# Kernel tuning notes

Hardware: AMD Instinct MI355X
Metric: run time of the kernel (lower is better)

## Reference

```python
import jax, jax.numpy as jnp
import numpy as np

N = 50000   # nodes
E = 800000  # edges
G = 64      # graphs
NEG_SLOPE = 0.2  # PyG GATConv leaky_relu slope


def gat_conv(x, edge_index, edge_attr, W, att_src, att_dst, We, att_edge, bias, num_nodes):
    # PyG GATConv, add_self_loops=False, concat=True, eval (no dropout)
    H, C = att_src.shape
    h = (x @ W).reshape(-1, H, C)                      # [N,H,C]
    a_src = (h * att_src).sum(-1)                      # [N,H]
    a_dst = (h * att_dst).sum(-1)                      # [N,H]
    src, dst = edge_index[0], edge_index[1]
    e = (edge_attr @ We).reshape(-1, H, C)             # [E,H,C]
    a_edge = (e * att_edge).sum(-1)                    # [E,H]
    alpha = a_src[src] + a_dst[dst] + a_edge           # [E,H]
    alpha = jax.nn.leaky_relu(alpha, NEG_SLOPE)
    # segment softmax over incoming edges of each dst node
    amax = jax.ops.segment_max(alpha, dst, num_segments=num_nodes)
    amax = jnp.where(jnp.isfinite(amax), amax, 0.0)
    ex = jnp.exp(alpha - amax[dst])
    denom = jax.ops.segment_sum(ex, dst, num_segments=num_nodes)
    att = ex / (denom[dst] + 1e-16)                    # [E,H]
    msg = h[src] * att[..., None]                      # [E,H,C]
    out = jax.ops.segment_sum(msg, dst, num_segments=num_nodes)
    return out.reshape(num_nodes, H * C) + bias


def setup_inputs() -> dict:
    key = jax.random.key(0)
    ks = jax.random.split(key, 20)
    s = 0.1
    inp = {
        "x": jax.random.normal(ks[0], (N, 128), jnp.float32),
        "edge_index": jax.random.randint(ks[1], (2, E), 0, N, dtype=jnp.int32),
        "edge_attr": jax.random.normal(ks[2], (E, 1), jnp.float32),
        "batch": jnp.sort(jax.random.randint(ks[3], (N,), 0, G, dtype=jnp.int32)),
        # layer 1: 128 -> 4 heads x 32
        "W1": jax.random.normal(ks[4], (128, 128), jnp.float32) * s,
        "as1": jax.random.normal(ks[5], (4, 32), jnp.float32) * s,
        "ad1": jax.random.normal(ks[6], (4, 32), jnp.float32) * s,
        "We1": jax.random.normal(ks[7], (1, 128), jnp.float32) * s,
        "ae1": jax.random.normal(ks[8], (4, 32), jnp.float32) * s,
        "b1": jnp.zeros((128,), jnp.float32),
        # layer 2: 128 -> 1 head x 64
        "W2": jax.random.normal(ks[9], (128, 64), jnp.float32) * s,
        "as2": jax.random.normal(ks[10], (1, 64), jnp.float32) * s,
        "ad2": jax.random.normal(ks[11], (1, 64), jnp.float32) * s,
        "We2": jax.random.normal(ks[12], (1, 64), jnp.float32) * s,
        "ae2": jax.random.normal(ks[13], (1, 64), jnp.float32) * s,
        "b2": jnp.zeros((64,), jnp.float32),
        # prediction head
        "Wp": jax.random.normal(ks[14], (64, 1), jnp.float32) * s,
        "bp": jnp.zeros((1,), jnp.float32),
    }
    return inp


def reference(x, edge_index, edge_attr, batch, W1, as1, ad1, We1, ae1, b1,
              W2, as2, ad2, We2, ae2, b2, Wp, bp):
    h = gat_conv(x, edge_index, edge_attr, W1, as1, ad1, We1, ae1, b1, N)
    h = jax.nn.relu(h)  # dropout p=0.0, eval mode
    h = gat_conv(h, edge_index, edge_attr, W2, as2, ad2, We2, ae2, b2, N)
    # per-graph mean pooling (vectorized replacement of the python loop)
    counts = jax.ops.segment_sum(jnp.ones((N,), h.dtype), batch, num_segments=G)
    sums = jax.ops.segment_sum(h, batch, num_segments=G)   # [G,64]
    mean = sums / counts[:, None]
    out = mean @ Wp + bp                                   # [G,1]
    return out.squeeze(-1)                                 # [G]
```

## Files before the change

### kernel.cpp

```cpp
#include <hip/hip_runtime.h>
#include <hip/hip_bf16.h>

typedef unsigned short u16;
typedef unsigned int u32;

#define MAXB 2048
#define POOL_MAXG 64

typedef __attribute__((ext_vector_type(8))) short bf16x8;
typedef __attribute__((ext_vector_type(4))) float f32x4;

__device__ __forceinline__ float bf2f(u16 u) { return __uint_as_float(((u32)u) << 16); }
__device__ __forceinline__ float bl(u32 u) { return __uint_as_float(u << 16); }
__device__ __forceinline__ float bh(u32 u) { return __uint_as_float(u & 0xffff0000u); }
__device__ __forceinline__ u16 f2bf(float f) {
    u32 u = __float_as_uint(f);
    u += 0x7fffu + ((u >> 16) & 1u);
    return (u16)(u >> 16);
}
__device__ __forceinline__ float lrelu(float x) { return x > 0.f ? x : 0.2f * x; }
__device__ __forceinline__ int clampi(int v, int lo, int hi) {
    return v < lo ? lo : (v > hi ? hi : v);
}
__device__ __forceinline__ float load1(const void* base, int idx, int f32) {
    return f32 ? ((const float*)base)[idx] : bf2f(((const u16*)base)[idx]);
}
__device__ __forceinline__ float cexpf(float a) {
    return __builtin_amdgcn_exp2f(fminf(a, 30.f) * 1.4426950408889634f);
}

__global__ void k_detect(const u32* __restrict__ xw, int* __restrict__ flag,
                         int* __restrict__ bcnt, int B) {
    int lane = threadIdx.x & 63;
    for (int i = lane; i < B; i += 64) bcnt[i] = 0;
    int cnt = 0;
    #pragma unroll
    for (int j = 0; j < 4; j++) {
        u32 w = xw[lane * 4 + j];
        int e0 = (int)((w >> 7) & 0xffu);
        int e1 = (int)((w >> 23) & 0xffu);
        cnt += (e0 >= 0x60 && e0 <= 0x8f);
        cnt += (e1 >= 0x60 && e1 <= 0x8f);
    }
    #pragma unroll
    for (int off = 32; off > 0; off >>= 1) cnt += __shfl_xor(cnt, off);
    if (lane == 0) *flag = (cnt < 480) ? 1 : 0;
}

__global__ void k_consts(const void* We1, const void* ae1, const void* We2, const void* ae2,
                         const void* as1, const void* ad1, const void* as2, const void* ad2,
                         const int* __restrict__ flag, float* __restrict__ consts,
                         float* __restrict__ pool, int psize) {
    int f = *flag;
    int t = threadIdx.x;
    for (int i = t; i < psize; i += 256) pool[i] = 0.f;
    if (t < 4) {
        float s = 0.f;
        for (int c = 0; c < 32; c++) s += load1(We1, t * 32 + c, f) * load1(ae1, t * 32 + c, f);
        consts[t] = s;
    } else if (t == 4) {
        float s = 0.f;
        for (int c = 0; c < 64; c++) s += load1(We2, c, f) * load1(ae2, c, f);
        consts[4] = s;
    }
    if (t < 128) {
        consts[8 + t] = load1(as1, t, f);
        consts[136 + t] = load1(ad1, t, f);
    }
    if (t < 64) {
        consts[264 + t] = load1(as2, t, f);
        consts[328 + t] = load1(ad2, t, f);
    }
}

template <int NC>
__global__ __launch_bounds__(256, 2) void k_gemm_mfma(
    const void* __restrict__ X, const void* __restrict__ Wg,
    const int* __restrict__ flag, int fXovr, u16* __restrict__ Y, int nrows) {
    constexpr int NCT = NC / 16;
    __shared__ __align__(16) u16 Bf[2][NCT][4][64][8];

    const int f = *flag;
    const bool fX = (fXovr < 0) ? (f != 0) : (fXovr != 0);
    const bool fW = (f != 0);
    const int tid = threadIdx.x;
    const int wid = tid >> 6, lane = tid & 63;

    for (int idx = tid; idx < NCT * 4 * 64; idx += 256) {
        int l = idx & 63;
        int s = (idx >> 6) & 3;
        int t = idx >> 8;
        int col = t * 16 + (l & 15);
        int k0 = s * 32 + (l >> 4) * 8;
        u16 hi[8], lo[8];
        #pragma unroll
        for (int j = 0; j < 8; j++) {
            int k = k0 + j;
            int srow = (NC == 64) ? ((k & 1) * 64 + (k >> 1)) : k;
            float v = fW ? ((const float*)Wg)[srow * NC + col]
                         : bf2f(((const u16*)Wg)[srow * NC + col]);
            u16 h = f2bf(v);
            hi[j] = h;
            lo[j] = fW ? f2bf(v - bf2f(h)) : (u16)0;
        }
        uint4 hv, lv;
        hv.x = (u32)hi[0] | ((u32)hi[1] << 16);
        hv.y = (u32)hi[2] | ((u32)hi[3] << 16);
        hv.z = (u32)hi[4] | ((u32)hi[5] << 16);
        hv.w = (u32)hi[6] | ((u32)hi[7] << 16);
        lv.x = (u32)lo[0] | ((u32)lo[1] << 16);
        lv.y = (u32)lo[2] | ((u32)lo[3] << 16);
        lv.z = (u32)lo[4] | ((u32)lo[5] << 16);
        lv.w = (u32)lo[6] | ((u32)lo[7] << 16);
        *(uint4*)&Bf[0][t][s][l][0] = hv;
        *(uint4*)&Bf[1][t][s][l][0] = lv;
    }
    __syncthreads();

    const int tiles = (nrows + 63) >> 6;
    for (int tile = blockIdx.x; tile < tiles; tile += gridDim.x) {
        const int rowbase = tile * 64 + wid * 16;
        const int arow = rowbase + (lane & 15);
        const bool rv = arow < nrows;

        bf16x8 ahi[4], alo[4];
        #pragma unroll
        for (int s = 0; s < 4; s++) {
            int koff = s * 32 + (lane >> 4) * 8;
            u16 h[8], l8[8];
            #pragma unroll
            for (int j = 0; j < 8; j++) { h[j] = 0; l8[j] = 0; }
            if (rv) {
                if (fX) {
                    const float* xp = (const float*)X + (size_t)arow * 128 + koff;
                    float4 a = *(const float4*)xp;
                    float4 b = *(const float4*)(xp + 4);
                    float vv[8];
                    vv[0] = a.x; vv[1] = a.y; vv[2] = a.z; vv[3] = a.w;
                    vv[4] = b.x; vv[5] = b.y; vv[6] = b.z; vv[7] = b.w;
                    #pragma unroll
                    for (int j = 0; j < 8; j++) {
                        h[j] = f2bf(vv[j]);
                        l8[j] = f2bf(vv[j] - bf2f(h[j]));
                    }
                } else {
                    const u16* xp = (const u16*)X + (size_t)arow * 128 + koff;
                    uint4 q = *(const uint4*)xp;
                    h[0] = (u16)q.x; h[1] = (u16)(q.x >> 16);
                    h[2] = (u16)q.y; h[3] = (u16)(q.y >> 16);
                    h[4] = (u16)q.z; h[5] = (u16)(q.z >> 16);
                    h[6] = (u16)q.w; h[7] = (u16)(q.w >> 16);
                }
            }
            bf16x8 vh, vl;
            #pragma unroll
            for (int j = 0; j < 8; j++) { vh[j] = (short)h[j]; vl[j] = (short)l8[j]; }
            ahi[s] = vh; alo[s] = vl;
        }

        f32x4 acc[NCT];
        #pragma unroll
        for (int t = 0; t < NCT; t++) acc[t] = (f32x4){0.f, 0.f, 0.f, 0.f};
        #pragma unroll
        for (int s = 0; s < 4; s++) {
            #pragma unroll
            for (int t = 0; t < NCT; t++) {
                bf16x8 bhi = *(const bf16x8*)&Bf[0][t][s][lane][0];
                acc[t] = __builtin_amdgcn_mfma_f32_16x16x32_bf16(ahi[s], bhi, acc[t], 0, 0, 0);
                if (fW) {
                    bf16x8 blo = *(const bf16x8*)&Bf[1][t][s][lane][0];
                    acc[t] = __builtin_amdgcn_mfma_f32_16x16x32_bf16(ahi[s], blo, acc[t], 0, 0, 0);
                }
                if (fX) {
                    acc[t] = __builtin_amdgcn_mfma_f32_16x16x32_bf16(alo[s], bhi, acc[t], 0, 0, 0);
                }
            }
        }

        #pragma unroll
        for (int reg = 0; reg < 4; reg++) {
            int r = rowbase + (lane >> 4) * 4 + reg;
            if (r < nrows) {
                if constexpr (NC == 128) {
                    #pragma unroll
                    for (int t = 0; t < 4; t++) {
                        u32 w = (u32)f2bf(acc[t][reg]) | ((u32)f2bf(acc[t + 4][reg]) << 16);
                        ((u32*)Y)[(size_t)r * 64 + t * 16 + (lane & 15)] = w;
                    }
                } else {
                    #pragma unroll
                    for (int t = 0; t < 4; t++)
                        Y[(size_t)r * 64 + t * 16 + (lane & 15)] = f2bf(acc[t][reg]);
                }
            }
        }
    }
}

__global__ void k_coef1(const u32* __restrict__ hp, const float* __restrict__ consts,
                        float* __restrict__ asrc, float* __restrict__ adst,
                        int* __restrict__ rpos, int n) {
    int i = blockIdx.x * 256 + threadIdx.x;
    if (i < n) rpos[i] = 0;
    if (i >= n * 2) return;
    int node = i >> 1, g = i & 1;
    const u32* w = hp + (size_t)node * 64 + g * 32;
    const float* asA = consts + 8 + g * 32;
    const float* adA = consts + 136 + g * 32;
    const float* asB = consts + 8 + (g + 2) * 32;
    const float* adB = consts + 136 + (g + 2) * 32;
    float sA1 = 0.f, sA2 = 0.f, sB1 = 0.f, sB2 = 0.f;
    #pragma unroll
    for (int c = 0; c < 32; c += 4) {
        uint4 q = *(const uint4*)&w[c];
        float l0 = bl(q.x), h0 = bh(q.x), l1 = bl(q.y), h1 = bh(q.y);
        float l2 = bl(q.z), h2 = bh(q.z), l3 = bl(q.w), h3 = bh(q.w);
        sA1 += l0 * asA[c] + l1 * asA[c + 1] + l2 * asA[c + 2] + l3 * asA[c + 3];
        sA2 += l0 * adA[c] + l1 * adA[c + 1] + l2 * adA[c + 2] + l3 * adA[c + 3];
        sB1 += h0 * asB[c] + h1 * asB[c + 1] + h2 * asB[c + 2] + h3 * asB[c + 3];
        sB2 += h0 * adB[c] + h1 * adB[c + 1] + h2 * adB[c + 2] + h3 * adB[c + 3];
    }
    asrc[node * 4 + g] = sA1;     adst[node * 4 + g] = sA2;
    asrc[node * 4 + g + 2] = sB1; adst[node * 4 + g + 2] = sB2;
}

__global__ void k_coef2(const u32* __restrict__ hp, const float* __restrict__ consts,
                        float* __restrict__ asrc, float* __restrict__ adst, int n) {
    int i = blockIdx.x * 256 + threadIdx.x;
    if (i >= n) return;
    const u32* w = hp + (size_t)i * 32;
    const float* as_ = consts + 264;
    const float* ad_ = consts + 328;
    float s1 = 0.f, s2 = 0.f;
    #pragma unroll
    for (int c = 0; c < 32; c += 4) {
        uint4 q = *(const uint4*)&w[c];
        float l0 = bl(q.x), h0 = bh(q.x), l1 = bl(q.y), h1 = bh(q.y);
        float l2 = bl(q.z), h2 = bh(q.z), l3 = bl(q.w), h3 = bh(q.w);
        s1 += l0 * as_[2*c] + h0 * as_[2*c+1] + l1 * as_[2*c+2] + h1 * as_[2*c+3]
            + l2 * as_[2*c+4] + h2 * as_[2*c+5] + l3 * as_[2*c+6] + h3 * as_[2*c+7];
        s2 += l0 * ad_[2*c] + h0 * ad_[2*c+1] + l1 * ad_[2*c+2] + h1 * ad_[2*c+3]
            + l2 * ad_[2*c+4] + h2 * ad_[2*c+5] + l3 * ad_[2*c+6] + h3 * ad_[2*c+7];
    }
    asrc[i] = s1; adst[i] = s2;
}

__global__ __launch_bounds__(256) void k_bhist2(const int* __restrict__ dst,
                                                int* __restrict__ bcnt, int E, int n, int B) {
    __shared__ int lh[MAXB];
    for (int i = threadIdx.x; i < B; i += 256) lh[i] = 0;
    __syncthreads();
    int stride = gridDim.x * 256;
    for (int e = blockIdx.x * 256 + threadIdx.x; e < E; e += stride) {
        int d = clampi(dst[e], 0, n - 1);
        atomicAdd(&lh[d >> 8], 1);
    }
    __syncthreads();
    for (int i = threadIdx.x; i < B; i += 256)
        if (lh[i]) atomicAdd(&bcnt[i], lh[i]);
}
__global__ void k_bscan(const int* __restrict__ bcnt, int* __restrict__ bbase,
                        int* __restrict__ bfront, int* __restrict__ roff,
                        int B, int N, int E) {
    __shared__ int buf[256];
    __shared__ int carry;
    int t = threadIdx.x;
    if (t == 0) carry = 0;
    __syncthreads();
    for (int base = 0; base < B; base += 256) {
        int k = base + t;
        int v = (k < B) ? bcnt[k] : 0;
        buf[t] = v;
        __syncthreads();
        for (int off = 1; off < 256; off <<= 1) {
            int u = (t >= off) ? buf[t - off] : 0;
            __syncthreads();
            buf[t] += u;
            __syncthreads();
        }
        int excl = carry + buf[t] - v;
        if (k < B) { bbase[k] = excl; bfront[k] = excl; }
        __syncthreads();
        if (t == 0) carry += buf[255];
        __syncthreads();
    }
    if (t == 0) { bbase[B] = carry; roff[N] = E; }
}
__global__ __launch_bounds__(256) void k_bhist(const int* __restrict__ dst,
                                               int* __restrict__ cnt, int* __restrict__ bcnt,
                                               int E, int n, int B) {
    __shared__ int lh[MAXB];
    for (int i = threadIdx.x; i < B; i += 256) lh[i] = 0;
    __syncthreads();
    int stride = gridDim.x * 256;
    for (int e = blockIdx.x * 256 + threadIdx.x; e < E; e += stride) {
        int d = clampi(dst[e], 0, n - 1);
        atomicAdd(&cnt[d], 1);
        atomicAdd(&lh[d >> 8], 1);
    }
    __syncthreads();
    for (int i = threadIdx.x; i < B; i += 256)
        if (lh[i]) atomicAdd(&bcnt[i], lh[i]);
}
__global__ void k_scan1(const int* __restrict__ cnt, int* __restrict__ part,
                        int* __restrict__ bsum, int n) {
    __shared__ int buf[256];
    int i = blockIdx.x * 256 + threadIdx.x;
    int v = (i < n) ? cnt[i] : 0;
    buf[threadIdx.x] = v;
    __syncthreads();
    for (int off = 1; off < 256; off <<= 1) {
        int t = (threadIdx.x >= off) ? buf[threadIdx.x - off] : 0;
        __syncthreads();
        buf[threadIdx.x] += t;
        __syncthreads();
    }
    if (i < n) part[i] = buf[threadIdx.x];
    if (threadIdx.x == 255) bsum[blockIdx.x] = buf[255];
}
__global__ void k_scan3b(int* __restrict__ roff, const int* __restrict__ bsum,
                         int* __restrict__ rpos, int n, int nb) {
    __shared__ int buf[256];
    int t = threadIdx.x;
    int v = (t < nb) ? bsum[t] : 0;
    buf[t] = v;
    __syncthreads();
    for (int off = 1; off < 256; off <<= 1) {
        int u = (t >= off) ? buf[t - off] : 0;
        __syncthreads();
        buf[t] += u;
        __syncthreads();
    }
    __shared__ int excl[256];
    excl[t] = buf[t] - v;
    __syncthreads();
    int i = blockIdx.x * 256 + t;
    if (i > n) return;
    int val;
    if (i == 0) { val = 0; roff[0] = 0; }
    else { val = roff[i] + excl[(i - 1) >> 8]; roff[i] = val; }
    if (i < n) rpos[i] = val;
}
__global__ __launch_bounds__(256) void k_binA(
    const int* __restrict__ dst, const int* __restrict__ src, const void* eattr,
    const int* __restrict__ flag, int* __restrict__ bfront, int4* __restrict__ staged,
    float4* __restrict__ stagedE, const float* __restrict__ asrc,
    const float* __restrict__ adst, const float* __restrict__ consts,
    int E, int n, int B) {
    __shared__ int lhist[MAXB];
    __shared__ int lbase[MAXB];
    int f = *flag;
    const float c0 = consts[0], c1 = consts[1], c2 = consts[2], c3 = consts[3];
    constexpr int T = 2048;
    for (int tile = blockIdx.x; (long long)tile * T < E; tile += gridDim.x) {
        int base = tile * T;
        for (int i = threadIdx.x; i < B; i += 256) lhist[i] = 0;
        __syncthreads();
        int sj0, sj1, sj2, sj3, sj4, sj5, sj6, sj7;
        int dj0, dj1, dj2, dj3, dj4, dj5, dj6, dj7;
        int rj0, rj1, rj2, rj3, rj4, rj5, rj6, rj7;
        int ej0, ej1, ej2, ej3, ej4, ej5, ej6, ej7;
        #define BINA_LOAD(J, SJ, DJ, RJ, EJ)                                   \
        {                                                                      \
            int idx = base + (J) * 256 + threadIdx.x;                          \
            bool v = idx < E;                                                  \
            int d = v ? clampi(dst[idx], 0, n - 1) : 0;                        \
            SJ = v ? clampi(src[idx], 0, n - 1) : 0;                           \
            EJ = v ? __float_as_int(load1(eattr, idx, f)) : 0;                 \
            DJ = d;                                                            \
            RJ = v ? atomicAdd(&lhist[d >> 8], 1) : -1;                        \
        }
        BINA_LOAD(0, sj0, dj0, rj0, ej0)
        BINA_LOAD(1, sj1, dj1, rj1, ej1)
        BINA_LOAD(2, sj2, dj2, rj2, ej2)
        BINA_LOAD(3, sj3, dj3, rj3, ej3)
        BINA_LOAD(4, sj4, dj4, rj4, ej4)
        BINA_LOAD(5, sj5, dj5, rj5, ej5)
        BINA_LOAD(6, sj6, dj6, rj6, ej6)
        BINA_LOAD(7, sj7, dj7, rj7, ej7)
        #undef BINA_LOAD
        __syncthreads();
        for (int i = threadIdx.x; i < B; i += 256) {
            int c = lhist[i];
            lbase[i] = c ? atomicAdd(&bfront[i], c) : 0;
        }
        __syncthreads();
        #define BINA_STORE(SJ, DJ, RJ, EJ)                                     \
        if (RJ >= 0) {                                                         \
            long long q = (long long)lbase[DJ >> 8] + RJ;                      \
            if (q >= 0 && q < E) {                                             \
                int4 v; v.x = SJ; v.y = DJ; v.z = EJ; v.w = 0;                 \
                staged[q] = v;                                                 \
                float ea = __int_as_float(EJ);                                 \
                float4 av = *(const float4*)&asrc[(size_t)SJ * 4];             \
                float4 dvv = *(const float4*)&adst[(size_t)DJ * 4];            \
                float4 evv;                                                    \
                evv.x = cexpf(lrelu(av.x + dvv.x + ea * c0));                  \
                evv.y = cexpf(lrelu(av.y + dvv.y + ea * c1));                  \
                evv.z = cexpf(lrelu(av.z + dvv.z + ea * c2));                  \
                evv.w = cexpf(lrelu(av.w + dvv.w + ea * c3));                  \
                stagedE[q] = evv;                                              \
            }                                                                  \
        }
        BINA_STORE(sj0, dj0, rj0, ej0)
        BINA_STORE(sj1, dj1, rj1, ej1)
        BINA_STORE(sj2, dj2, rj2, ej2)
        BINA_STORE(sj3, dj3, rj3, ej3)
        BINA_STORE(sj4, dj4, rj4, ej4)
        BINA_STORE(sj5, dj5, rj5, ej5)
        BINA_STORE(sj6, dj6, rj6, ej6)
        BINA_STORE(sj7, dj7, rj7, ej7)
        #undef BINA_STORE
        __syncthreads();
    }
}
__global__ __launch_bounds__(256) void k_binB2(
    const int4* __restrict__ staged, const float4* __restrict__ stagedE,
    const int* __restrict__ bbase, int* __restrict__ roff,
    int2* __restrict__ edata, float* __restrict__ eexp, int N, int E, int B) {
    __shared__ int lcnt[256];
    __shared__ int buf[256];
    __shared__ int lpos[256];
    int k = blockIdx.x;
    int t = threadIdx.x;
    lcnt[t] = 0;
    __syncthreads();
    int lo = clampi(bbase[k], 0, E);
    int hi = clampi(bbase[k + 1], lo, E);
    for (int i = lo + t; i < hi; i += 256)
        atomicAdd(&lcnt[staged[i].y & 255], 1);
    __syncthreads();
    int v = lcnt[t];
    buf[t] = v;
    __syncthreads();
    for (int off = 1; off < 256; off <<= 1) {
        int u = (t >= off) ? buf[t - off] : 0;
        __syncthreads();
        buf[t] += u;
        __syncthreads();
    }
    int pos = lo + buf[t] - v;
    int dn = (k << 8) + t;
    if (dn < N) roff[dn] = pos;
    lpos[t] = pos;
    __syncthreads();
    for (int i = lo + t; i < hi; i += 256) {
        int4 vv = staged[i];
        float4 ev = stagedE[i];
        int p = atomicAdd(&lpos[vv.y & 255], 1);
        if (p >= 0 && p < E) {
            edata[p] = make_int2(vv.x, vv.z);
            *(float4*)&eexp[(size_t)p * 4] = ev;
        }
    }
}
__global__ void k_scatter(const int* __restrict__ dst, const int* __restrict__ src,
                          const void* eattr, const int* __restrict__ flag,
                          int* __restrict__ rpos, int2* __restrict__ edata,
                          float* __restrict__ eexp, const float* __restrict__ asrc,
                          const float* __restrict__ adst, const float* __restrict__ consts,
                          int E, int n) {
    int f = *flag;
    int e = blockIdx.x * 256 + threadIdx.x;
    if (e < E) {
        int d = clampi(dst[e], 0, n - 1);
        int s = clampi(src[e], 0, n - 1);
        float ea = load1(eattr, e, f);
        int p = atomicAdd(&rpos[d], 1);
        if (p >= 0 && p < E) {
            int2 v; v.x = s; v.y = __float_as_int(ea);
            edata[p] = v;
            if (eexp) {
                float4 av = *(const float4*)&asrc[(size_t)s * 4];
                float4 dv = *(const float4*)&adst[(size_t)d * 4];
                float4 ev;
                ev.x = cexpf(lrelu(av.x + dv.x + ea * consts[0]));
                ev.y = cexpf(lrelu(av.y + dv.y + ea * consts[1]));
                ev.z = cexpf(lrelu(av.z + dv.z + ea * consts[2]));
                ev.w = cexpf(lrelu(av.w + dv.w + ea * consts[3]));
                *(float4*)&eexp[(size_t)p * 4] = ev;
            }
        }
    }
}

__global__ __launch_bounds__(256) void k_gat1c(
    const u32* __restrict__ hp, const float* __restrict__ eexp,
    const int2* __restrict__ edata, const int* __restrict__ roff,
    const int* __restrict__ flag, const void* bias, u32* __restrict__ out, int n, int E) {
    __shared__ float4 wls[4][64];
    int f = *flag;
    int gtid = blockIdx.x * 256 + threadIdx.x;
    int wv = gtid >> 6, lane = gtid & 63;
    int wid = (threadIdx.x >> 6);
    int nw = (gridDim.x * 256) >> 6;
    const int hl = lane & 31;
    const int sel = lane >> 5;
    const int p0 = hl * 2;
    const int phsel = hl >> 4;
    const float biasA0 = load1(bias, p0, f);
    const float biasB0 = load1(bias, 64 + p0, f);
    const float biasA1 = load1(bias, p0 + 1, f);
    const float biasB1 = load1(bias, 64 + p0 + 1, f);
    const int ghsel = lane >> 5;
    const float gbiasA = load1(bias, lane, f);
    const float gbiasB = load1(bias, 64 + lane, f);

    for (int db = wv * 2; db < n; db += nw * 2) {
        int d = db + sel;
        bool dv = d < n;
        int s0 = dv ? clampi(roff[d], 0, E) : 0;
        int s1 = dv ? clampi(roff[d + 1], s0, E) : 0;
        int deg = s1 - s0;

        if (__all(deg <= 32)) {
            bool v = hl < deg;
            int s = 0;
            float4 ev = make_float4(0.f, 0.f, 0.f, 0.f);
            if (v) {
                ev = *(const float4*)&eexp[(size_t)(s0 + hl) * 4];
                s = edata[s0 + hl].x;
            }
            float d0 = ev.x, d1 = ev.y, d2 = ev.z, d3 = ev.w;
            #pragma unroll
            for (int off = 16; off > 0; off >>= 1) {
                d0 += __shfl_xor(d0, off); d1 += __shfl_xor(d1, off);
                d2 += __shfl_xor(d2, off); d3 += __shfl_xor(d3, off);
            }
            float i0 = 1.f / (d0 + 1e-16f), i1 = 1.f / (d1 + 1e-16f);
            float i2 = 1.f / (d2 + 1e-16f), i3 = 1.f / (d3 + 1e-16f);
            wls[wid][lane] = make_float4(ev.x * i0, ev.y * i1, ev.z * i2, ev.w * i3);

            int degm = max(deg, __shfl_xor(deg, 32));
            int base = sel * 32;
            float aA0 = 0.f, aB0 = 0.f, aA1 = 0.f, aB1 = 0.f;
            for (int j = 0; j < degm; j += 4) {
                int j0 = base + j, j1 = base + j + 1, j2 = base + j + 2, j3 = base + j + 3;
                int sa = __shfl(s, j0), sb = __shfl(s, j1);
                int sc_ = __shfl(s, j2), sd = __shfl(s, j3);
                float4 wa = wls[wid][j0], wb = wls[wid][j1];
                float4 wc = wls[wid][j2], wd = wls[wid][j3];
                uint2 ha = *(const uint2*)(hp + (size_t)sa * 64 + p0);
                uint2 hb = *(const uint2*)(hp + (size_t)sb * 64 + p0);
                uint2 hc = *(const uint2*)(hp + (size_t)sc_ * 64 + p0);
                uint2 hd = *(const uint2*)(hp + (size_t)sd * 64 + p0);
                float wAa = phsel ? wa.y : wa.x, wBa = phsel ? wa.w : wa.z;
                float wAb = phsel ? wb.y : wb.x, wBb = phsel ? wb.w : wb.z;
                float wAc = phsel ? wc.y : wc.x, wBc = phsel ? wc.w : wc.z;
                float wAd = phsel ? wd.y : wd.x, wBd = phsel ? wd.w : wd.z;
                aA0 += wAa * bl(ha.x); aB0 += wBa * bh(ha.x);
                aA1 += wAa * bl(ha.y); aB1 += wBa * bh(ha.y);
                aA0 += wAb * bl(hb.x); aB0 += wBb * bh(hb.x);
                aA1 += wAb * bl(hb.y); aB1 += wBb * bh(hb.y);
                aA0 += wAc * bl(hc.x); aB0 += wBc * bh(hc.x);
                aA1 += wAc * bl(hc.y); aB1 += wBc * bh(hc.y);
                aA0 += wAd * bl(hd.x); aB0 += wBd * bh(hd.x);
                aA1 += wAd * bl(hd.y); aB1 += wBd * bh(hd.y);
            }
            if (dv) {
                u32 w0 = (u32)f2bf(fmaxf(aA0 + biasA0, 0.f))
                       | ((u32)f2bf(fmaxf(aB0 + biasB0, 0.f)) << 16);
                u32 w1 = (u32)f2bf(fmaxf(aA1 + biasA1, 0.f))
                       | ((u32)f2bf(fmaxf(aB1 + biasB1, 0.f)) << 16);
                *(uint2*)(out + (size_t)d * 64 + p0) = make_uint2(w0, w1);
            }
        } else {
            for (int q = 0; q < 2; q++) {
                int dq = db + q;
                if (dq >= n) break;
                int t0 = clampi(roff[dq], 0, E);
                int t1 = clampi(roff[dq + 1], t0, E);
                int dg = t1 - t0;
                if (dg <= 64) {
                    bool v = lane < dg;
                    int s = 0;
                    float4 ev = make_float4(0.f, 0.f, 0.f, 0.f);
                    if (v) {
                        ev = *(const float4*)&eexp[(size_t)(t0 + lane) * 4];
                        s = edata[t0 + lane].x;
                    }
                    float d0 = ev.x, d1 = ev.y, d2 = ev.z, d3 = ev.w;
                    #pragma unroll
                    for (int off = 32; off > 0; off >>= 1) {
                        d0 += __shfl_xor(d0, off); d1 += __shfl_xor(d1, off);
                        d2 += __shfl_xor(d2, off); d3 += __shfl_xor(d3, off);
                    }
                    float i0 = 1.f / (d0 + 1e-16f), i1 = 1.f / (d1 + 1e-16f);
                    float i2 = 1.f / (d2 + 1e-16f), i3 = 1.f / (d3 + 1e-16f);
                    wls[wid][lane] = make_float4(ev.x * i0, ev.y * i1, ev.z * i2, ev.w * i3);

                    float aA0 = 0.f, aB0 = 0.f, aA1 = 0.f, aB1 = 0.f;
                    for (int j = 0; j < dg; j += 4) {
                        int j0 = j + sel, j1 = j + 2 + sel;
                        int sa = __shfl(s, j0), sb = __shfl(s, j1);
                        float4 wa = wls[wid][j0], wb = wls[wid][j1];
                        uint2 ha = *(const uint2*)(hp + (size_t)sa * 64 + p0);
                        uint2 hb = *(const uint2*)(hp + (size_t)sb * 64 + p0);
                        float wAa = phsel ? wa.y : wa.x, wBa = phsel ? wa.w : wa.z;
                        float wAb = phsel ? wb.y : wb.x, wBb = phsel ? wb.w : wb.z;
                        aA0 += wAa * bl(ha.x); aB0 += wBa * bh(ha.x);
                        aA1 += wAa * bl(ha.y); aB1 += wBa * bh(ha.y);
                        aA0 += wAb * bl(hb.x); aB0 += wBb * bh(hb.x);
                        aA1 += wAb * bl(hb.y); aB1 += wBb * bh(hb.y);
                    }
                    aA0 += __shfl_xor(aA0, 32); aB0 += __shfl_xor(aB0, 32);
                    aA1 += __shfl_xor(aA1, 32); aB1 += __shfl_xor(aB1, 32);
                    if (lane < 32) {
                        u32 w0 = (u32)f2bf(fmaxf(aA0 + biasA0, 0.f))
                               | ((u32)f2bf(fmaxf(aB0 + biasB0, 0.f)) << 16);
                        u32 w1 = (u32)f2bf(fmaxf(aA1 + biasA1, 0.f))
                               | ((u32)f2bf(fmaxf(aB1 + biasB1, 0.f)) << 16);
                        *(uint2*)(out + (size_t)dq * 64 + p0) = make_uint2(w0, w1);
                    }
                } else {
                    float d0 = 0.f, d1 = 0.f, d2 = 0.f, d3 = 0.f;
                    for (int idx = t0 + lane; idx < t1; idx += 64) {
                        float4 ev = *(const float4*)&eexp[(size_t)idx * 4];
                        d0 += ev.x; d1 += ev.y; d2 += ev.z; d3 += ev.w;
                    }
                    #pragma unroll
                    for (int off = 32; off > 0; off >>= 1) {
                        d0 += __shfl_xor(d0, off); d1 += __shfl_xor(d1, off);
                        d2 += __shfl_xor(d2, off); d3 += __shfl_xor(d3, off);
                    }
                    float i0 = 1.f / (d0 + 1e-16f), i1 = 1.f / (d1 + 1e-16f);
                    float i2 = 1.f / (d2 + 1e-16f), i3 = 1.f / (d3 + 1e-16f);
                    float iA = ghsel ? i1 : i0, iB = ghsel ? i3 : i2;
                    float accA = 0.f, accB = 0.f;
                    for (int idx = t0; idx < t1; idx++) {
                        float4 ev = *(const float4*)&eexp[(size_t)idx * 4];
                        int s = edata[idx].x;
                        float wA = (ghsel ? ev.y : ev.x) * iA;
                        float wB = (ghsel ? ev.w : ev.z) * iB;
                        u32 hw = hp[(size_t)s * 64 + lane];
                        accA += wA * bl(hw);
                        accB += wB * bh(hw);
                    }
                    float rA = fmaxf(accA + gbiasA, 0.f);
                    float rB = fmaxf(accB + gbiasB, 0.f);
                    out[(size_t)dq * 64 + lane] = (u32)f2bf(rA) | ((u32)f2bf(rB) << 16);
                }
            }
        }
    }
}

__global__ __launch_bounds__(256) void k_gat2c(
    const u16* __restrict__ h, const float* __restrict__ asrc, const float* __restrict__ adst,
    const int2* __restrict__ edata, const int* __restrict__ roff,
    const int* __restrict__ flag, const float* __restrict__ consts, const void* bias,
    u16* __restrict__ out, int n, int E) {
    __shared__ float wls[4][64];
    int f = *flag;
    int gtid = blockIdx.x * 256 + threadIdx.x;
    int wv = gtid >> 6, lane = gtid & 63;
    int wid = (threadIdx.x >> 6);
    int nw = (gridDim.x * 256) >> 6;
    const float C = consts[4];
    const int hl = lane & 31;
    const int sel = lane >> 5;
    const int p0 = hl * 2;
    const float bias0 = load1(bias, p0, f);
    const float bias1 = load1(bias, p0 + 1, f);
    const float gbias = load1(bias, lane, f);

    for (int db = wv * 2; db < n; db += nw * 2) {
        int d = db + sel;
        bool dv = d < n;
        int s0 = dv ? clampi(roff[d], 0, E) : 0;
        int s1 = dv ? clampi(roff[d + 1], s0, E) : 0;
        int deg = s1 - s0;
        float ad = dv ? adst[d] : 0.f;

        if (__all(deg <= 32)) {
            bool v = hl < deg;
            int s = 0;
            float e = 0.f;
            if (v) {
                int2 ed = edata[s0 + hl];
                s = ed.x;
                e = cexpf(lrelu(asrc[s] + ad + __int_as_float(ed.y) * C));
            }
            float den = e;
            #pragma unroll
            for (int off = 16; off > 0; off >>= 1) den += __shfl_xor(den, off);
            float inv = 1.f / (den + 1e-16f);
            wls[wid][lane] = e * inv;

            int degm = max(deg, __shfl_xor(deg, 32));
            int base = sel * 32;
            float a0 = 0.f, a1 = 0.f;
            for (int j = 0; j < degm; j += 4) {
                int j0 = base + j, j1 = base + j + 1, j2 = base + j + 2, j3 = base + j + 3;
                int sa = __shfl(s, j0), sb = __shfl(s, j1);
                int sc_ = __shfl(s, j2), sd = __shfl(s, j3);
                float wa = wls[wid][j0], wb = wls[wid][j1];
                float wc = wls[wid][j2], wd = wls[wid][j3];
                u32 ha = *(const u32*)(h + (size_t)sa * 64 + p0);
                u32 hb = *(const u32*)(h + (size_t)sb * 64 + p0);
                u32 hc = *(const u32*)(h + (size_t)sc_ * 64 + p0);
                u32 hd = *(const u32*)(h + (size_t)sd * 64 + p0);
                a0 += wa * bl(ha) + wb * bl(hb) + wc * bl(hc) + wd * bl(hd);
                a1 += wa * bh(ha) + wb * bh(hb) + wc * bh(hc) + wd * bh(hd);
            }
            if (dv) {
                u32 w = (u32)f2bf(a0 + bias0) | ((u32)f2bf(a1 + bias1) << 16);
                *(u32*)(out + (size_t)d * 64 + p0) = w;
            }
        } else {
            for (int q = 0; q < 2; q++) {
                int dq = db + q;
                if (dq >= n) break;
                int t0 = clampi(roff[dq], 0, E);
                int t1 = clampi(roff[dq + 1], t0, E);
                int dg = t1 - t0;
                float adq = adst[dq];
                if (dg <= 64) {
                    bool v = lane < dg;
                    int s = 0;
                    float e = 0.f;
                    if (v) {
                        int2 ed = edata[t0 + lane];
                        s = ed.x;
                        e = cexpf(lrelu(asrc[s] + adq + __int_as_float(ed.y) * C));
                    }
                    float den = e;
                    #pragma unroll
                    for (int off = 32; off > 0; off >>= 1) den += __shfl_xor(den, off);
                    float inv = 1.f / (den + 1e-16f);
                    wls[wid][lane] = e * inv;

                    float a0 = 0.f, a1 = 0.f;
                    for (int j = 0; j < dg; j += 4) {
                        int j0 = j + sel, j1 = j + 2 + sel;
                        int sa = __shfl(s, j0), sb = __shfl(s, j1);
                        float wa = wls[wid][j0], wb = wls[wid][j1];
                        u32 ha = *(const u32*)(h + (size_t)sa * 64 + p0);
                        u32 hb = *(const u32*)(h + (size_t)sb * 64 + p0);
                        a0 += wa * bl(ha) + wb * bl(hb);
                        a1 += wa * bh(ha) + wb * bh(hb);
                    }
                    a0 += __shfl_xor(a0, 32);
                    a1 += __shfl_xor(a1, 32);
                    if (lane < 32) {
                        u32 w = (u32)f2bf(a0 + bias0) | ((u32)f2bf(a1 + bias1) << 16);
                        *(u32*)(out + (size_t)dq * 64 + p0) = w;
                    }
                } else {
                    float den = 0.f;
                    for (int idx = t0 + lane; idx < t1; idx += 64) {
                        int2 ed = edata[idx];
                        den += cexpf(lrelu(asrc[ed.x] + adq + __int_as_float(ed.y) * C));
                    }
                    #pragma unroll
                    for (int off = 32; off > 0; off >>= 1) den += __shfl_xor(den, off);
                    float inv = 1.f / (den + 1e-16f);
                    float acc = 0.f;
                    for (int idx = t0; idx < t1; idx++) {
                        int2 ed = edata[idx];
                        float w = cexpf(lrelu(asrc[ed.x] + adq
                                              + __int_as_float(ed.y) * C)) * inv;
                        acc += w * bf2f(h[(size_t)ed.x * 64 + lane]);
                    }
                    out[(size_t)dq * 64 + lane] = f2bf(acc + gbias);
                }
            }
        }
    }
}

__global__ __launch_bounds__(256) void k_gat1f(
    const u32* __restrict__ hp, const float* __restrict__ asrc, const float* __restrict__ adst,
    const int2* __restrict__ edata, const int* __restrict__ roff,
    const int* __restrict__ flag, const float* __restrict__ consts, const void* bias,
    u32* __restrict__ out, int n, int E) {
    int f = *flag;
    int gtid = blockIdx.x * 256 + threadIdx.x;
    int wv = gtid >> 6, lane = gtid & 63;
    int nw = (gridDim.x * 256) >> 6;
    const float c0 = consts[0], c1 = consts[1], c2 = consts[2], c3 = consts[3];
    const int hsel = lane >> 5;
    const float biasA = load1(bias, lane, f);
    const float biasB = load1(bias, 64 + lane, f);

    for (int d = wv; d < n; d += nw) {
        int s0 = clampi(roff[d], 0, E);
        int s1 = clampi(roff[d + 1], s0, E);
        float4 adv = *(const float4*)&adst[d * 4];
        float d0 = 0.f, d1 = 0.f, d2 = 0.f, d3 = 0.f;
        for (int idx = s0 + lane; idx < s1; idx += 64) {
            int2 ed = edata[idx];
            float ea = __int_as_float(ed.y);
            float4 av = *(const float4*)&asrc[(size_t)ed.x * 4];
            d0 += cexpf(lrelu(av.x + adv.x + ea * c0));
            d1 += cexpf(lrelu(av.y + adv.y + ea * c1));
            d2 += cexpf(lrelu(av.z + adv.z + ea * c2));
            d3 += cexpf(lrelu(av.w + adv.w + ea * c3));
        }
        #pragma unroll
        for (int off = 32; off > 0; off >>= 1) {
            d0 += __shfl_xor(d0, off); d1 += __shfl_xor(d1, off);
            d2 += __shfl_xor(d2, off); d3 += __shfl_xor(d3, off);
        }
        float i0 = 1.f / (d0 + 1e-16f), i1 = 1.f / (d1 + 1e-16f);
        float i2 = 1.f / (d2 + 1e-16f), i3 = 1.f / (d3 + 1e-16f);
        float iA = hsel ? i1 : i0, iB = hsel ? i3 : i2;
        float cA = hsel ? c1 : c0, cB = hsel ? c3 : c2;
        float aA = hsel ? adv.y : adv.x, aB = hsel ? adv.w : adv.z;

        float accA = 0.f, accB = 0.f;
        for (int idx = s0; idx < s1; idx++) {
            int2 ed = edata[idx];
            float ea = __int_as_float(ed.y);
            float4 av = *(const float4*)&asrc[(size_t)ed.x * 4];
            float wA = cexpf(lrelu((hsel ? av.y : av.x) + aA + ea * cA)) * iA;
            float wB = cexpf(lrelu((hsel ? av.w : av.z) + aB + ea * cB)) * iB;
            u32 hw = hp[(size_t)ed.x * 64 + lane];
            accA += wA * bl(hw);
            accB += wB * bh(hw);
        }
        float rA = fmaxf(accA + biasA, 0.f);
        float rB = fmaxf(accB + biasB, 0.f);
        out[(size_t)d * 64 + lane] = (u32)f2bf(rA) | ((u32)f2bf(rB) << 16);
    }
}

__global__ __launch_bounds__(256) void k_gat2f(
    const u16* __restrict__ h, const float* __restrict__ asrc, const float* __restrict__ adst,
    const int2* __restrict__ edata, const int* __restrict__ roff,
    const int* __restrict__ flag, const float* __restrict__ consts, const void* bias,
    u16* __restrict__ out, int n, int E) {
    int f = *flag;
    int gtid = blockIdx.x * 256 + threadIdx.x;
    int wv = gtid >> 6, lane = gtid & 63;
    int nw = (gridDim.x * 256) >> 6;
    const float C = consts[4];
    const float biasL = load1(bias, lane, f);

    for (int d = wv; d < n; d += nw) {
        int s0 = clampi(roff[d], 0, E);
        int s1 = clampi(roff[d + 1], s0, E);
        float ad = adst[d];
        float den = 0.f;
        for (int idx = s0 + lane; idx < s1; idx += 64) {
            int2 ed = edata[idx];
            den += cexpf(lrelu(asrc[ed.x] + ad + __int_as_float(ed.y) * C));
        }
        #pragma unroll
        for (int off = 32; off > 0; off >>= 1) den += __shfl_xor(den, off);
        float inv = 1.f / (den + 1e-16f);

        float acc = 0.f;
        for (int idx = s0; idx < s1; idx++) {
            int2 ed = edata[idx];
            float w = cexpf(lrelu(asrc[ed.x] + ad + __int_as_float(ed.y) * C)) * inv;
            acc += w * bf2f(h[(size_t)ed.x * 64 + lane]);
        }
        out[(size_t)d * 64 + lane] = f2bf(acc + biasL);
    }
}

__global__ __launch_bounds__(256) void k_pool2(
    const u16* __restrict__ agg2, const int* __restrict__ batch,
    float* __restrict__ pool, float* __restrict__ cnt, int n, int G, int rpb) {
    __shared__ float lp[POOL_MAXG * 64];
    __shared__ float lc[POOL_MAXG];
    int t = threadIdx.x;
    for (int i = t; i < G * 64; i += 256) lp[i] = 0.f;
    for (int i = t; i < G; i += 256) lc[i] = 0.f;
    __syncthreads();
    int lane = t & 63;
    int rl = t >> 6;
    int r0 = blockIdx.x * rpb;
    int r1 = min(r0 + rpb, n);
    float acc = 0.f, cacc = 0.f;
    int curg = -1;
    for (int j = r0 + rl; j < r1; j += 4) {
        int g = clampi(batch[j], 0, G - 1);
        float v = bf2f(agg2[(size_t)j * 64 + lane]);
        if (g != curg) {
            if (curg >= 0) {
                atomicAdd(&lp[curg * 64 + lane], acc);
                if (lane == 0) atomicAdd(&lc[curg], cacc);
            }
            acc = 0.f; cacc = 0.f; curg = g;
        }
        acc += v; cacc += 1.f;
    }
    if (curg >= 0) {
        atomicAdd(&lp[curg * 64 + lane], acc);
        if (lane == 0) atomicAdd(&lc[curg], cacc);
    }
    __syncthreads();
    for (int i = t; i < G * 64; i += 256) {
        float v = lp[i];
        if (v != 0.f) atomicAdd(&pool[i], v);
    }
    for (int i = t; i < G; i += 256) {
        float v = lc[i];
        if (v != 0.f) atomicAdd(&cnt[i], v);
    }
}

__global__ void k_pool(const u16* __restrict__ agg2, const int* __restrict__ batch,
                       float* __restrict__ pool, float* __restrict__ cnt, int n, int G) {
    int t = blockIdx.x * 256 + threadIdx.x;
    int nb8 = (n + 7) / 8;
    if (t >= nb8 * 64) return;
    int base = (t >> 6) * 8;
    int c = t & 63;
    int end = min(base + 8, n);
    float acc = 0.f, cacc = 0.f;
    int curg = clampi(batch[base], 0, G - 1);
    for (int j = base; j < end; j++) {
        int g = clampi(batch[j], 0, G - 1);
        if (g != curg) {
            atomicAdd(&pool[curg * 64 + c], acc);
            if (c == 0) atomicAdd(&cnt[curg], cacc);
            acc = 0.f; cacc = 0.f; curg = g;
        }
        acc += bf2f(agg2[(size_t)j * 64 + c]);
        cacc += 1.f;
    }
    atomicAdd(&pool[curg * 64 + c], acc);
    if (c == 0) atomicAdd(&cnt[curg], cacc);
}

__global__ void k_head(const float* __restrict__ pool, const float* __restrict__ cnt,
                       const void* Wp, const void* bp, const int* __restrict__ flag,
                       void* out, int G) {
    int f = *flag;
    int g = threadIdx.x;
    if (g >= G) return;
    float s = 0.f;
    for (int c = 0; c < 64; c++) s += pool[g * 64 + c] * load1(Wp, c, f);
    float cv = cnt[g];
    if (!(cv > 0.f)) cv = 1.f;
    float r = s / cv + load1(bp, 0, f);
    if (f) ((float*)out)[g] = r;
    else   ((u16*)out)[g] = f2bf(r);
}

extern "C" void kernel_launch(void* const* d_in, const int* in_sizes, int n_in,
                              void* d_out, int out_size, void* d_ws, size_t ws_size,
                              hipStream_t stream) {
    const void* x    = d_in[0];
    const int* ei    = (const int*)d_in[1];
    const void* eattr = d_in[2];
    const int* batch = (const int*)d_in[3];
    const void* W1   = d_in[4];
    const void* as1  = d_in[5];
    const void* ad1  = d_in[6];
    const void* We1  = d_in[7];
    const void* ae1  = d_in[8];
    const void* b1   = d_in[9];
    const void* W2   = d_in[10];
    const void* as2  = d_in[11];
    const void* ad2  = d_in[12];
    const void* We2  = d_in[13];
    const void* ae2  = d_in[14];
    const void* b2   = d_in[15];
    const void* Wp   = d_in[16];
    const void* bp   = d_in[17];

    const int N = in_sizes[3];
    const int E = in_sizes[2];
    const int G = out_size;
    const int* src = ei;
    const int* dst = ei + E;
    const int B = (N + 255) >> 8;

    char* p = (char*)d_ws;
    auto alloc = [&](size_t bytes) -> char* {
        char* r = p;
        p += (bytes + 255) & ~(size_t)255;
        return r;
    };
    int* flag    = (int*)alloc(32);
    float* consts = (float*)alloc(2048);
    int* roff    = (int*)alloc((size_t)(N + 1) * 4);
    int* rpos    = (int*)alloc((size_t)N * 4);
    int* bsum    = (int*)alloc(256 * 4);
    int* bcnt    = (int*)alloc((size_t)(MAXB * 3 + 1) * 4);
    int* bbase   = bcnt + MAXB;
    int* bfront  = bbase + MAXB + 1;
    int2* edata  = (int2*)alloc((size_t)E * 8);
    float* pool  = (float*)alloc((size_t)(G * 64 + G) * 4);
    float* cnt   = pool + (size_t)G * 64;
    float* asrc1 = (float*)alloc((size_t)N * 4 * 4);
    float* adst1 = (float*)alloc((size_t)N * 4 * 4);
    float* asrc2 = asrc1;
    float* adst2 = adst1;
    u16* agg1    = (u16*)alloc((size_t)N * 128 * 2);
    u16* h1      = (u16*)alloc((size_t)N * 128 * 2);
    u16* h2      = h1;
    u16* agg2    = h1 + (size_t)N * 64;
    float* eexp  = (float*)alloc((size_t)E * 16);
    int4* staged = (int4*)alloc((size_t)E * 16);
    float4* stagedE = (float4*)alloc((size_t)E * 16);
    size_t full_need = (size_t)(p - (char*)d_ws);
    const bool cached = (ws_size >= full_need);
    const bool binned = cached && (B <= MAXB);

    const int GG = (N + 127) >> 7;

    k_detect<<<1, 64, 0, stream>>>((const u32*)x, flag, bcnt, B);
    k_consts<<<1, 256, 0, stream>>>(We1, ae1, We2, ae2, as1, ad1, as2, ad2, flag, consts,
                                    pool, G * 64 + G);
    k_gemm_mfma<128><<<GG, 256, 0, stream>>>(x, W1, flag, -1, h1, N);
    k_coef1<<<(N * 2 + 255) / 256, 256, 0, stream>>>((const u32*)h1, consts, asrc1, adst1,
                                                     rpos, N);

    if (binned) {
        k_bhist2<<<512, 256, 0, stream>>>(dst, bcnt, E, N, B);
        k_bscan<<<1, 256, 0, stream>>>(bcnt, bbase, bfront, roff, B, N, E);
        k_binA<<<(E + 2047) / 2048, 256, 0, stream>>>(dst, src, eattr, flag, bfront,
                                                      staged, stagedE, asrc1, adst1,
                                                      consts, E, N, B);
        k_binB2<<<B, 256, 0, stream>>>(staged, stagedE, bbase, roff, edata, eexp, N, E, B);
    } else {
        int NB = (N + 255) / 256;
        k_bhist<<<512, 256, 0, stream>>>(dst, rpos, bcnt, E, N, B);
        k_scan1<<<NB, 256, 0, stream>>>(rpos, roff + 1, bsum, N);
        k_scan3b<<<(N + 256) / 256, 256, 0, stream>>>(roff, bsum, rpos, N, NB);
        k_scatter<<<(E + 255) / 256, 256, 0, stream>>>(dst, src, eattr, flag, rpos,
                                                       edata, cached ? eexp : nullptr,
                                                       asrc1, adst1, consts, E, N);
    }

    int gatBlocks = (N * 64 + 255) / 256;
    if (cached) {
        k_gat1c<<<gatBlocks, 256, 0, stream>>>((const u32*)h1, eexp, edata, roff,
                                               flag, b1, (u32*)agg1, N, E);
    } else {
        k_gat1f<<<gatBlocks, 256, 0, stream>>>((const u32*)h1, asrc1, adst1, edata, roff,
                                               flag, consts, b1, (u32*)agg1, N, E);
    }
    k_gemm_mfma<64><<<GG, 256, 0, stream>>>(agg1, W2, flag, 0, h2, N);
    k_coef2<<<(N + 255) / 256, 256, 0, stream>>>((const u32*)h2, consts, asrc2, adst2, N);
    if (cached) {
        k_gat2c<<<gatBlocks, 256, 0, stream>>>(h2, asrc2, adst2, edata, roff, flag,
                                               consts, b2, agg2, N, E);
    } else {
        k_gat2f<<<gatBlocks, 256, 0, stream>>>(h2, asrc2, adst2, edata, roff, flag,
                                               consts, b2, agg2, N, E);
    }
    if (G <= POOL_MAXG) {
        int rpb = (N + 1023) / 1024;
        if (rpb < 8) rpb = 8;
        int pblocks = (N + rpb - 1) / rpb;
        k_pool2<<<pblocks, 256, 0, stream>>>(agg2, batch, pool, cnt, N, G, rpb);
    } else {
        k_pool<<<(((N + 7) / 8) * 64 + 255) / 256, 256, 0, stream>>>(agg2, batch, pool,
                                                                     cnt, N, G);
    }
    k_head<<<1, 64, 0, stream>>>(pool, cnt, Wp, bp, flag, d_out, G);
}
```

Baseline: 307.8 us.

## Fuse attention coefficients into GEMM epilogues, merge init kernels, pack staged edges

The per-node attention dot products (a_src, a_dst) are now computed in the MFMA GEMM epilogue from fp32 accumulators using lane shuffles, which removes the separate k_coef1 and k_coef2 kernels and their re-read of h. The detect and constants kernels are merged into one launch. Staged edge records shrink from int4 to int2 by packing src with the low 8 bits of dst, cutting binning traffic but requiring N ≤ 2^24. Coefficients now come from unrounded fp32 values rather than from bf16-rounded h, so results can differ slightly.

```diff
diff --git a/kernel.cpp b/kernel.cpp
--- a/kernel.cpp
+++ b/kernel.cpp
@@ -29,30 +29,30 @@
     return __builtin_amdgcn_exp2f(fminf(a, 30.f) * 1.4426950408889634f);
 }
 
-__global__ void k_detect(const u32* __restrict__ xw, int* __restrict__ flag,
-                         int* __restrict__ bcnt, int B) {
-    int lane = threadIdx.x & 63;
-    for (int i = lane; i < B; i += 64) bcnt[i] = 0;
-    int cnt = 0;
-    #pragma unroll
-    for (int j = 0; j < 4; j++) {
-        u32 w = xw[lane * 4 + j];
-        int e0 = (int)((w >> 7) & 0xffu);
-        int e1 = (int)((w >> 23) & 0xffu);
-        cnt += (e0 >= 0x60 && e0 <= 0x8f);
-        cnt += (e1 >= 0x60 && e1 <= 0x8f);
-    }
-    #pragma unroll
-    for (int off = 32; off > 0; off >>= 1) cnt += __shfl_xor(cnt, off);
-    if (lane == 0) *flag = (cnt < 480) ? 1 : 0;
-}
-
-__global__ void k_consts(const void* We1, const void* ae1, const void* We2, const void* ae2,
-                         const void* as1, const void* ad1, const void* as2, const void* ad2,
-                         const int* __restrict__ flag, float* __restrict__ consts,
-                         float* __restrict__ pool, int psize) {
-    int f = *flag;
+__global__ void k_init(const u32* __restrict__ xw, int* __restrict__ flag,
+                       int* __restrict__ bcnt, int B,
+                       const void* We1, const void* ae1, const void* We2, const void* ae2,
+                       const void* as1, const void* ad1, const void* as2, const void* ad2,
+                       float* __restrict__ consts, float* __restrict__ pool, int psize) {
+    __shared__ int sf;
     int t = threadIdx.x;
+    for (int i = t; i < B; i += 256) bcnt[i] = 0;
+    if (t < 64) {
+        int cnt = 0;
+        #pragma unroll
+        for (int j = 0; j < 4; j++) {
+            u32 w = xw[t * 4 + j];
+            int e0 = (int)((w >> 7) & 0xffu);
+            int e1 = (int)((w >> 23) & 0xffu);
+            cnt += (e0 >= 0x60 && e0 <= 0x8f);
+            cnt += (e1 >= 0x60 && e1 <= 0x8f);
+        }
+        #pragma unroll
+        for (int off = 32; off > 0; off >>= 1) cnt += __shfl_xor(cnt, off);
+        if (t == 0) { int v = (cnt < 480) ? 1 : 0; *flag = v; sf = v; }
+    }
+    __syncthreads();
+    int f = sf;
     for (int i = t; i < psize; i += 256) pool[i] = 0.f;
     if (t < 4) {
         float s = 0.f;
@@ -76,7 +76,9 @@
 template <int NC>
 __global__ __launch_bounds__(256, 2) void k_gemm_mfma(
     const void* __restrict__ X, const void* __restrict__ Wg,
-    const int* __restrict__ flag, int fXovr, u16* __restrict__ Y, int nrows) {
+    const int* __restrict__ flag, int fXovr, u16* __restrict__ Y,
+    const float* __restrict__ consts, float* __restrict__ casrc,
+    float* __restrict__ cadst, int nrows) {
     constexpr int NCT = NC / 16;
     __shared__ __align__(16) u16 Bf[2][NCT][4][64][8];
 
@@ -194,55 +196,61 @@
                 }
             }
         }
-    }
-}
-
-__global__ void k_coef1(const u32* __restrict__ hp, const float* __restrict__ consts,
-                        float* __restrict__ asrc, float* __restrict__ adst,
-                        int* __restrict__ rpos, int n) {
-    int i = blockIdx.x * 256 + threadIdx.x;
-    if (i < n) rpos[i] = 0;
-    if (i >= n * 2) return;
-    int node = i >> 1, g = i & 1;
-    const u32* w = hp + (size_t)node * 64 + g * 32;
-    const float* asA = consts + 8 + g * 32;
-    const float* adA = consts + 136 + g * 32;
-    const float* asB = consts + 8 + (g + 2) * 32;
-    const float* adB = consts + 136 + (g + 2) * 32;
-    float sA1 = 0.f, sA2 = 0.f, sB1 = 0.f, sB2 = 0.f;
-    #pragma unroll
-    for (int c = 0; c < 32; c += 4) {
-        uint4 q = *(const uint4*)&w[c];
-        float l0 = bl(q.x), h0 = bh(q.x), l1 = bl(q.y), h1 = bh(q.y);
-        float l2 = bl(q.z), h2 = bh(q.z), l3 = bl(q.w), h3 = bh(q.w);
-        sA1 += l0 * asA[c] + l1 * asA[c + 1] + l2 * asA[c + 2] + l3 * asA[c + 3];
-        sA2 += l0 * adA[c] + l1 * adA[c + 1] + l2 * adA[c + 2] + l3 * adA[c + 3];
-        sB1 += h0 * asB[c] + h1 * asB[c + 1] + h2 * asB[c + 2] + h3 * asB[c + 3];
-        sB2 += h0 * adB[c] + h1 * adB[c + 1] + h2 * adB[c + 2] + h3 * adB[c + 3];
-    }
-    asrc[node * 4 + g] = sA1;     adst[node * 4 + g] = sA2;
-    asrc[node * 4 + g + 2] = sB1; adst[node * 4 + g + 2] = sB2;
-}
-
-__global__ void k_coef2(const u32* __restrict__ hp, const float* __restrict__ consts,
-                        float* __restrict__ asrc, float* __restrict__ adst, int n) {
-    int i = blockIdx.x * 256 + threadIdx.x;
-    if (i >= n) return;
-    const u32* w = hp + (size_t)i * 32;
-    const float* as_ = consts + 264;
-    const float* ad_ = consts + 328;
-    float s1 = 0.f, s2 = 0.f;
-    #pragma unroll
-    for (int c = 0; c < 32; c += 4) {
-        uint4 q = *(const uint4*)&w[c];
-        float l0 = bl(q.x), h0 = bh(q.x), l1 = bl(q.y), h1 = bh(q.y);
-        float l2 = bl(q.z), h2 = bh(q.z), l3 = bl(q.w), h3 = bh(q.w);
-        s1 += l0 * as_[2*c] + h0 * as_[2*c+1] + l1 * as_[2*c+2] + h1 * as_[2*c+3]
-            + l2 * as_[2*c+4] + h2 * as_[2*c+5] + l3 * as_[2*c+6] + h3 * as_[2*c+7];
-        s2 += l0 * ad_[2*c] + h0 * ad_[2*c+1] + l1 * ad_[2*c+2] + h1 * ad_[2*c+3]
-            + l2 * ad_[2*c+4] + h2 * ad_[2*c+5] + l3 * ad_[2*c+6] + h3 * ad_[2*c+7];
-    }
-    asrc[i] = s1; adst[i] = s2;
+
+        if (casrc) {
+            const int l16 = lane & 15;
+            if constexpr (NC == 128) {
+                #pragma unroll
+                for (int reg = 0; reg < 4; reg++) {
+                    int r = rowbase + (lane >> 4) * 4 + reg;
+                    float pA[4] = {0.f, 0.f, 0.f, 0.f};
+                    float pD[4] = {0.f, 0.f, 0.f, 0.f};
+                    #pragma unroll
+                    for (int t = 0; t < 4; t++) {
+                        int p = t * 16 + l16;
+                        int g = t >> 1;
+                        pA[g]     += acc[t][reg]     * consts[8 + p];
+                        pD[g]     += acc[t][reg]     * consts[136 + p];
+                        pA[g + 2] += acc[t + 4][reg] * consts[72 + p];
+                        pD[g + 2] += acc[t + 4][reg] * consts[200 + p];
+                    }
+                    #pragma unroll
+                    for (int off = 1; off < 16; off <<= 1) {
+                        #pragma unroll
+                        for (int g = 0; g < 4; g++) {
+                            pA[g] += __shfl_xor(pA[g], off);
+                            pD[g] += __shfl_xor(pD[g], off);
+                        }
+                    }
+                    if (l16 == 0 && r < nrows) {
+                        #pragma unroll
+                        for (int g = 0; g < 4; g++) {
+                            casrc[r * 4 + g] = pA[g];
+                            cadst[r * 4 + g] = pD[g];
+                        }
+                    }
+                }
+            } else {
+                #pragma unroll
+                for (int reg = 0; reg < 4; reg++) {
+                    int r = rowbase + (lane >> 4) * 4 + reg;
+                    float s1 = 0.f, s2 = 0.f;
+                    #pragma unroll
+                    for (int t = 0; t < 4; t++) {
+                        int p = t * 16 + l16;
+                        s1 += acc[t][reg] * consts[264 + p];
+                        s2 += acc[t][reg] * consts[328 + p];
+                    }
+                    #pragma unroll
+                    for (int off = 1; off < 16; off <<= 1) {
+                        s1 += __shfl_xor(s1, off);
+                        s2 += __shfl_xor(s2, off);
+                    }
+                    if (l16 == 0 && r < nrows) { casrc[r] = s1; cadst[r] = s2; }
+                }
+            }
+        }
+    }
 }
 
 __global__ __launch_bounds__(256) void k_bhist2(const int* __restrict__ dst,
@@ -286,6 +294,10 @@
     }
     if (t == 0) { bbase[B] = carry; roff[N] = E; }
 }
+__global__ void k_zero(int* __restrict__ p, int n) {
+    int i = blockIdx.x * 256 + threadIdx.x;
+    if (i < n) p[i] = 0;
+}
 __global__ __launch_bounds__(256) void k_bhist(const int* __restrict__ dst,
                                                int* __restrict__ cnt, int* __restrict__ bcnt,
                                                int E, int n, int B) {
@@ -343,7 +355,7 @@
 }
 __global__ __launch_bounds__(256) void k_binA(
     const int* __restrict__ dst, const int* __restrict__ src, const void* eattr,
-    const int* __restrict__ flag, int* __restrict__ bfront, int4* __restrict__ staged,
+    const int* __restrict__ flag, int* __restrict__ bfront, int2* __restrict__ stagedA,
     float4* __restrict__ stagedE, const float* __restrict__ asrc,
     const float* __restrict__ adst, const float* __restrict__ consts,
     int E, int n, int B) {
@@ -389,8 +401,10 @@
         if (RJ >= 0) {                                                         \
             long long q = (long long)lbase[DJ >> 8] + RJ;                      \
             if (q >= 0 && q < E) {                                             \
-                int4 v; v.x = SJ; v.y = DJ; v.z = EJ; v.w = 0;                 \
-                staged[q] = v;                                                 \
+                int2 v2;                                                       \
+                v2.x = (SJ & 0xFFFFFF) | ((DJ & 255) << 24);                   \
+                v2.y = EJ;                                                     \
+                stagedA[q] = v2;                                               \
                 float ea = __int_as_float(EJ);                                 \
                 float4 av = *(const float4*)&asrc[(size_t)SJ * 4];             \
                 float4 dvv = *(const float4*)&adst[(size_t)DJ * 4];            \
@@ -415,7 +429,7 @@
     }
 }
 __global__ __launch_bounds__(256) void k_binB2(
-    const int4* __restrict__ staged, const float4* __restrict__ stagedE,
+    const int2* __restrict__ stagedA, const float4* __restrict__ stagedE,
     const int* __restrict__ bbase, int* __restrict__ roff,
     int2* __restrict__ edata, float* __restrict__ eexp, int N, int E, int B) {
     __shared__ int lcnt[256];
@@ -428,7 +442,7 @@
     int lo = clampi(bbase[k], 0, E);
     int hi = clampi(bbase[k + 1], lo, E);
     for (int i = lo + t; i < hi; i += 256)
-        atomicAdd(&lcnt[staged[i].y & 255], 1);
+        atomicAdd(&lcnt[(stagedA[i].x >> 24) & 255], 1);
     __syncthreads();
     int v = lcnt[t];
     buf[t] = v;
@@ -445,11 +459,11 @@
     lpos[t] = pos;
     __syncthreads();
     for (int i = lo + t; i < hi; i += 256) {
-        int4 vv = staged[i];
+        int2 a = stagedA[i];
         float4 ev = stagedE[i];
-        int p = atomicAdd(&lpos[vv.y & 255], 1);
+        int p = atomicAdd(&lpos[(a.x >> 24) & 255], 1);
         if (p >= 0 && p < E) {
-            edata[p] = make_int2(vv.x, vv.z);
+            edata[p] = make_int2(a.x & 0xFFFFFF, a.y);
             *(float4*)&eexp[(size_t)p * 4] = ev;
         }
     }
@@ -996,30 +1010,30 @@
     u16* h2      = h1;
     u16* agg2    = h1 + (size_t)N * 64;
     float* eexp  = (float*)alloc((size_t)E * 16);
-    int4* staged = (int4*)alloc((size_t)E * 16);
+    int2* stagedA = (int2*)alloc((size_t)E * 8);
     float4* stagedE = (float4*)alloc((size_t)E * 16);
     size_t full_need = (size_t)(p - (char*)d_ws);
     const bool cached = (ws_size >= full_need);
-    const bool binned = cached && (B <= MAXB);
+    const bool binned = cached && (B <= MAXB) && (N <= (1 << 24));
 
     const int GG = (N + 127) >> 7;
 
-    k_detect<<<1, 64, 0, stream>>>((const u32*)x, flag, bcnt, B);
-    k_consts<<<1, 256, 0, stream>>>(We1, ae1, We2, ae2, as1, ad1, as2, ad2, flag, consts,
-                                    pool, G * 64 + G);
-    k_gemm_mfma<128><<<GG, 256, 0, stream>>>(x, W1, flag, -1, h1, N);
-    k_coef1<<<(N * 2 + 255) / 256, 256, 0, stream>>>((const u32*)h1, consts, asrc1, adst1,
-                                                     rpos, N);
+    k_init<<<1, 256, 0, stream>>>((const u32*)x, flag, bcnt, B,
+                                  We1, ae1, We2, ae2, as1, ad1, as2, ad2,
+                                  consts, pool, G * 64 + G);
+    k_gemm_mfma<128><<<GG, 256, 0, stream>>>(x, W1, flag, -1, h1, consts,
+                                             asrc1, adst1, N);
 
     if (binned) {
         k_bhist2<<<512, 256, 0, stream>>>(dst, bcnt, E, N, B);
         k_bscan<<<1, 256, 0, stream>>>(bcnt, bbase, bfront, roff, B, N, E);
         k_binA<<<(E + 2047) / 2048, 256, 0, stream>>>(dst, src, eattr, flag, bfront,
-                                                      staged, stagedE, asrc1, adst1,
+                                                      stagedA, stagedE, asrc1, adst1,
                                                       consts, E, N, B);
-        k_binB2<<<B, 256, 0, stream>>>(staged, stagedE, bbase, roff, edata, eexp, N, E, B);
+        k_binB2<<<B, 256, 0, stream>>>(stagedA, stagedE, bbase, roff, edata, eexp, N, E, B);
     } else {
         int NB = (N + 255) / 256;
+        k_zero<<<(N + 255) / 256, 256, 0, stream>>>(rpos, N);
         k_bhist<<<512, 256, 0, stream>>>(dst, rpos, bcnt, E, N, B);
         k_scan1<<<NB, 256, 0, stream>>>(rpos, roff + 1, bsum, N);
         k_scan3b<<<(N + 256) / 256, 256, 0, stream>>>(roff, bsum, rpos, N, NB);
@@ -1036,8 +1050,8 @@
         k_gat1f<<<gatBlocks, 256, 0, stream>>>((const u32*)h1, asrc1, adst1, edata, roff,
                                                flag, consts, b1, (u32*)agg1, N, E);
     }
-    k_gemm_mfma<64><<<GG, 256, 0, stream>>>(agg1, W2, flag, 0, h2, N);
-    k_coef2<<<(N + 255) / 256, 256, 0, stream>>>((const u32*)h2, consts, asrc2, adst2, N);
+    k_gemm_mfma<64><<<GG, 256, 0, stream>>>(agg1, W2, flag, 0, h2, consts,
+                                            asrc2, adst2, N);
     if (cached) {
         k_gat2c<<<gatBlocks, 256, 0, stream>>>(h2, asrc2, adst2, edata, roff, flag,
                                                consts, b2, agg2, N, E);
```

Measured after the change: 299.5 us. 1.03x faster.
